# Kernel optimization log

Hardware: AMD Instinct MI355X
Metric: run time of the kernel (lower is better)

## Reference

```python
import jax, jax.numpy as jnp
import numpy as np

EMB = 512
HEADS = 8
WINDOW = 128


def setup_inputs() -> dict:
    key = jax.random.key(0)
    ks = jax.random.split(key, 9)
    s = 1.0 / np.sqrt(EMB)
    x = jax.random.normal(ks[0], (2, 4096, EMB), dtype=jnp.float32)
    mk = lambda k: jax.random.uniform(k, (EMB, EMB), jnp.float32, -s, s)
    mb = lambda k: jax.random.uniform(k, (EMB,), jnp.float32, -s, s)
    return {
        "x": x,
        "Wq": mk(ks[1]), "bq": mb(ks[2]),
        "Wk": mk(ks[3]), "bk": mb(ks[4]),
        "Wv": mk(ks[5]), "bv": mb(ks[6]),
        "Wo": mk(ks[7]), "bo": mb(ks[8]),
    }


def _split_heads(y, b, n):
    # [b, n, emb] -> [b, h, n, d]
    return y.reshape(b, n, HEADS, EMB // HEADS).transpose(0, 2, 1, 3)


def reference(x, Wq, bq, Wk, bk, Wv, bv, Wo, bo):
    b, n, _ = x.shape
    q = _split_heads(x @ Wq.T + bq, b, n)
    k = _split_heads(x @ Wk.T + bk, b, n)
    v = _split_heads(x @ Wv.T + bv, b, n)
    energy = jnp.einsum('bhqd,bhkd->bhqk', q, k)  # [b,h,n,n]
    idx = jnp.arange(n)
    # banded mask: disallowed where |i - j| > window (matches torch loop)
    disallow = jnp.abs(idx[:, None] - idx[None, :]) > WINDOW
    fmin = jnp.float32(np.finfo(np.float32).min)
    energy = jnp.where(disallow[None, None], fmin, energy)
    att = jax.nn.softmax(energy / jnp.float32(np.sqrt(EMB)), axis=-1)
    out = jnp.einsum('bhql,bhld->bhqd', att, v)
    out = out.transpose(0, 2, 1, 3).reshape(b, n, EMB)
    return out @ Wo.T + bo
```

## Files before the change

kernel.cpp:

```cpp
#include <hip/hip_runtime.h>

#define EMB 512
#define HEADS 8
#define HD 64
#define NSEQ 4096
#define BATCH 2
#define WINDOW 128

typedef unsigned short u16;
typedef __attribute__((ext_vector_type(8))) short bf16x8;
typedef __attribute__((ext_vector_type(4))) float f32x4;

#define XS 4194304u
#define WS 262144u
#define BS 512u

__device__ __forceinline__ float bf2f(u16 u) {
    union { unsigned int i; float f; } x;
    x.i = ((unsigned int)u) << 16;
    return x.f;
}

__device__ __forceinline__ u16 f2bf(float f) {
    union { float f; unsigned int i; } x;
    x.f = f;
    unsigned int i = x.i;
    unsigned int lsb = (i >> 16) & 1u;
    i += 0x7fffu + lsb;
    return (u16)(i >> 16);
}

struct raw8 { uint4 lo, hi; };

__device__ __forceinline__ raw8 loadraw8(const void* base, size_t off, int isbf) {
    raw8 r;
    if (isbf) {
        r.lo = *(const uint4*)((const u16*)base + off);
    } else {
        const float* f = (const float*)base + off;
        r.lo = *(const uint4*)f;
        r.hi = *(const uint4*)(f + 4);
    }
    return r;
}

__device__ __forceinline__ uint4 cvt8(const raw8& r, int isbf) {
    if (isbf) return r.lo;
    const float* a = (const float*)&r.lo;
    const float* b = (const float*)&r.hi;
    uint4 o;
    o.x = (unsigned)f2bf(a[0]) | ((unsigned)f2bf(a[1]) << 16);
    o.y = (unsigned)f2bf(a[2]) | ((unsigned)f2bf(a[3]) << 16);
    o.z = (unsigned)f2bf(b[0]) | ((unsigned)f2bf(b[1]) << 16);
    o.w = (unsigned)f2bf(b[2]) | ((unsigned)f2bf(b[3]) << 16);
    return o;
}

__device__ __forceinline__ int probe_bf16(const void* p) {
    const int lane = threadIdx.x & 63;
    u16 w = ((const u16*)p)[lane * 2];
    int e = (w >> 7) & 0xff;
    bool sane = (w == 0) || (e >= 100 && e <= 140);
    unsigned long long m = __ballot(sane);
    return __popcll(m) >= 48;
}

__global__ __launch_bounds__(256)
void prepass(const void* __restrict__ x,
             const void* __restrict__ Wq, const void* __restrict__ bq,
             const void* __restrict__ Wk, const void* __restrict__ bk,
             const void* __restrict__ Wv, const void* __restrict__ bv,
             const void* __restrict__ Wo, const void* __restrict__ bo,
             u16* __restrict__ xb, u16* __restrict__ wb, u16* __restrict__ bb,
             int* __restrict__ flags)
{
    const int fx  = probe_bf16(x);
    const int fwq = probe_bf16(Wq), fbq = probe_bf16(bq);
    const int fwk = probe_bf16(Wk), fbk = probe_bf16(bk);
    const int fwv = probe_bf16(Wv), fbv = probe_bf16(bv);
    const int fwo = probe_bf16(Wo), fbo = probe_bf16(bo);
    if (blockIdx.x == 0 && threadIdx.x == 0) flags[0] = fx;

    size_t idx = ((size_t)blockIdx.x * 256 + threadIdx.x) * 8;
    const size_t T_X = XS, T_W = XS + 4 * (size_t)WS, T_ALL = T_W + 4 * (size_t)BS;
    if (idx >= T_ALL) return;

    const void* src; int fl; u16* dst; size_t off;
    if (idx < T_X) {
        src = x; fl = fx; dst = xb; off = idx;
    } else if (idx < T_W) {
        size_t w = idx - T_X;
        int wi = (int)(w / WS); off = w % WS;
        src = (wi == 0) ? Wq : (wi == 1) ? Wk : (wi == 2) ? Wv : Wo;
        fl  = (wi == 0) ? fwq : (wi == 1) ? fwk : (wi == 2) ? fwv : fwo;
        dst = wb + (size_t)wi * WS;
    } else {
        size_t b = idx - T_W;
        int bi = (int)(b / BS); off = b % BS;
        src = (bi == 0) ? bq : (bi == 1) ? bk : (bi == 2) ? bv : bo;
        fl  = (bi == 0) ? fbq : (bi == 1) ? fbk : (bi == 2) ? fbv : fbo;
        dst = bb + (size_t)bi * BS;
    }
    *(uint4*)(dst + off) = cvt8(loadraw8(src, off, fl), fl);
}

#define TP 136
__global__ __launch_bounds__(256)
void qkv_gemm(const u16* __restrict__ X, const u16* __restrict__ Wall,
              const u16* __restrict__ ball,
              u16* __restrict__ qo, u16* __restrict__ ko, u16* __restrict__ vo)
{
    __shared__ __align__(16) u16 SH[64 * TP];
    u16* As = SH;
    u16* Bs = SH + 4096;

    const int tid  = threadIdx.x;
    const int wave = tid >> 6;
    const int lane = tid & 63;
    const int quad = lane >> 4;
    const int l16  = lane & 15;
    const int wm = wave >> 1, wn = wave & 1;

    const int m0 = blockIdx.x * 128;
    const int by = blockIdx.y;
    const int wsel = by >> 2;
    const int n0 = (by & 3) * 128;

    const u16* W  = Wall + (size_t)wsel * WS;
    const u16* bi = ball + (size_t)wsel * BS;
    u16* out      = (wsel == 0) ? qo : (wsel == 1) ? ko : vo;
    const float oscale = (wsel == 0) ? 0.04419417382415922f : 1.0f;

    f32x4 acc[4][4];
#pragma unroll
    for (int i = 0; i < 4; ++i)
#pragma unroll
        for (int j = 0; j < 4; ++j)
            acc[i][j] = (f32x4){0.f, 0.f, 0.f, 0.f};

    const int c1 = tid, c2 = tid + 256;
    const int r1 = c1 >> 2, k1 = (c1 & 3) * 8;
    const int r2 = c2 >> 2, k2 = (c2 & 3) * 8;

    uint4 a1 = *(const uint4*)(X + (size_t)(m0 + r1) * EMB + k1);
    uint4 a2 = *(const uint4*)(X + (size_t)(m0 + r2) * EMB + k2);
    uint4 b1 = *(const uint4*)(W + (size_t)(n0 + r1) * EMB + k1);
    uint4 b2 = *(const uint4*)(W + (size_t)(n0 + r2) * EMB + k2);

    for (int kt = 0; kt < 16; ++kt) {
        __syncthreads();
        *(uint4*)&As[c1 * 8] = a1;
        *(uint4*)&As[c2 * 8] = a2;
        *(uint4*)&Bs[c1 * 8] = b1;
        *(uint4*)&Bs[c2 * 8] = b2;
        __syncthreads();

        if (kt < 15) {
            const int kk0 = (kt + 1) * 32;
            a1 = *(const uint4*)(X + (size_t)(m0 + r1) * EMB + kk0 + k1);
            a2 = *(const uint4*)(X + (size_t)(m0 + r2) * EMB + kk0 + k2);
            b1 = *(const uint4*)(W + (size_t)(n0 + r1) * EMB + kk0 + k1);
            b2 = *(const uint4*)(W + (size_t)(n0 + r2) * EMB + kk0 + k2);
        }

        bf16x8 af[4], bfr[4];
#pragma unroll
        for (int i = 0; i < 4; ++i)
            af[i] = *(const bf16x8*)&As[(wm * 64 + i * 16 + l16) * 32 + quad * 8];
#pragma unroll
        for (int j = 0; j < 4; ++j)
            bfr[j] = *(const bf16x8*)&Bs[(wn * 64 + j * 16 + l16) * 32 + quad * 8];
#pragma unroll
        for (int i = 0; i < 4; ++i)
#pragma unroll
            for (int j = 0; j < 4; ++j)
                acc[i][j] = __builtin_amdgcn_mfma_f32_16x16x32_bf16(af[i], bfr[j], acc[i][j], 0, 0, 0);
    }

    if (wsel != 2) {
#pragma unroll
        for (int j = 0; j < 4; ++j) {
            const int col = n0 + wn * 64 + j * 16 + l16;
            const float bv_ = bf2f(bi[col]);
            const int h = col >> 6, d = col & 63;
#pragma unroll
            for (int i = 0; i < 4; ++i) {
#pragma unroll
                for (int r = 0; r < 4; ++r) {
                    const int row = m0 + wm * 64 + i * 16 + quad * 4 + r;
                    const int b = row >> 12, n = row & 4095;
                    out[(((size_t)(b * HEADS + h) * NSEQ) + n) * HD + d] =
                        f2bf((acc[i][j][r] + bv_) * oscale);
                }
            }
        }
    } else {
        const int b = m0 >> 12;
        const int nbase = m0 & 4095;
#pragma unroll
        for (int half = 0; half < 2; ++half) {
            __syncthreads();
            if (wn == half) {
#pragma unroll
                for (int j = 0; j < 4; ++j) {
                    const int col = n0 + wn * 64 + j * 16 + l16;
                    const float bv_ = bf2f(bi[col]);
                    const int cl = j * 16 + l16;
#pragma unroll
                    for (int i = 0; i < 4; ++i)
#pragma unroll
                        for (int r = 0; r < 4; ++r) {
                            const int rowl = wm * 64 + i * 16 + quad * 4 + r;
                            SH[cl * TP + rowl] = f2bf(acc[i][j][r] + bv_);
                        }
                }
            }
            __syncthreads();
#pragma unroll
            for (int p = 0; p < 4; ++p) {
                const int idx  = tid + p * 256;
                const int dcol = idx >> 4;
                const int nch  = (idx & 15) * 8;
                uint4 val = *(const uint4*)&SH[dcol * TP + nch];
                const int col = n0 + half * 64 + dcol;
                const int h = col >> 6, d = col & 63;
                *(uint4*)(out + ((size_t)((b * HEADS + h) * HD + d)) * NSEQ + nbase + nch) = val;
            }
        }
    }
}

#define KP 72
__global__ __launch_bounds__(256)
void attn_mfma(const u16* __restrict__ q, const u16* __restrict__ k,
               const u16* __restrict__ v, u16* __restrict__ ao)
{
    __shared__ __align__(16) u16 Ks[64 * KP];
    __shared__ __align__(16) u16 Vt[64 * KP];

    const int tid  = threadIdx.x;
    const int wave = tid >> 6;
    const int lane = tid & 63;
    const int quad = lane >> 4;
    const int l16  = lane & 15;

    const int bh = blockIdx.y;
    const int q0 = blockIdx.x * 64;
    const int qw = q0 + wave * 16;
    const size_t base = (size_t)bh * NSEQ * HD;

    bf16x8 qa0 = *(const bf16x8*)(q + base + (size_t)(qw + l16) * HD + quad * 8);
    bf16x8 qa1 = *(const bf16x8*)(q + base + (size_t)(qw + l16) * HD + 32 + quad * 8);

    f32x4 O[4];
    float m_run = -1e30f, l_run = 0.f;
#pragma unroll
    for (int t = 0; t < 4; ++t) O[t] = (f32x4){0.f, 0.f, 0.f, 0.f};

    const int row_s[2] = { tid >> 3, (tid + 256) >> 3 };
    const int ch8      = (tid & 7) * 8;

    uint4 pkv[2], pvv[2];
    {
        const int kbase = q0 - 128;
        const int koff  = (kbase < 0) ? 0 : (kbase > NSEQ - 64 ? NSEQ - 64 : kbase);
#pragma unroll
        for (int s = 0; s < 2; ++s) {
            int kg = kbase + row_s[s];
            kg = (kg < 0) ? 0 : (kg > NSEQ - 1 ? NSEQ - 1 : kg);
            pkv[s] = *(const uint4*)(k + base + (size_t)kg * HD + ch8);
            pvv[s] = *(const uint4*)(v + base + (size_t)row_s[s] * NSEQ + koff + ch8);
        }
    }

    for (int c = 0; c < 5; ++c) {
        const int kbase = q0 - 128 + c * 64;

        __syncthreads();
#pragma unroll
        for (int s = 0; s < 2; ++s) {
            *(uint4*)&Ks[row_s[s] * KP + ch8] = pkv[s];
            *(uint4*)&Vt[row_s[s] * KP + ch8] = pvv[s];
        }
        __syncthreads();

        if (c < 4) {
            const int kb2  = kbase + 64;
            const int koff = (kb2 < 0) ? 0 : (kb2 > NSEQ - 64 ? NSEQ - 64 : kb2);
#pragma unroll
            for (int s = 0; s < 2; ++s) {
                int kg = kb2 + row_s[s];
                kg = (kg < 0) ? 0 : (kg > NSEQ - 1 ? NSEQ - 1 : kg);
                pkv[s] = *(const uint4*)(k + base + (size_t)kg * HD + ch8);
                pvv[s] = *(const uint4*)(v + base + (size_t)row_s[s] * NSEQ + koff + ch8);
            }
        }

        f32x4 sv[4];
#pragma unroll
        for (int t = 0; t < 4; ++t) {
            bf16x8 b0 = *(const bf16x8*)&Ks[(t * 16 + l16) * KP + quad * 8];
            bf16x8 b1 = *(const bf16x8*)&Ks[(t * 16 + l16) * KP + 32 + quad * 8];
            f32x4 sacc = (f32x4){0.f, 0.f, 0.f, 0.f};
            sacc = __builtin_amdgcn_mfma_f32_16x16x32_bf16(b0, qa0, sacc, 0, 0, 0);
            sacc = __builtin_amdgcn_mfma_f32_16x16x32_bf16(b1, qa1, sacc, 0, 0, 0);
            sv[t] = sacc;
        }

        const int iq = qw + l16;
#pragma unroll
        for (int t = 0; t < 4; ++t) {
#pragma unroll
            for (int r = 0; r < 4; ++r) {
                const int jg = kbase + t * 16 + quad * 4 + r;
                const bool jok = ((unsigned)jg) < (unsigned)NSEQ;
                const bool band = ((unsigned)(iq - jg + WINDOW)) <= (unsigned)(2 * WINDOW);
                if (!(jok && band)) sv[t][r] = -1e30f;
            }
        }

        float mnew = sv[0][0];
#pragma unroll
        for (int t = 0; t < 4; ++t)
#pragma unroll
            for (int r = 0; r < 4; ++r) mnew = fmaxf(mnew, sv[t][r]);
        mnew = fmaxf(mnew, __shfl_xor(mnew, 16, 64));
        mnew = fmaxf(mnew, __shfl_xor(mnew, 32, 64));

        const float mi = fmaxf(m_run, mnew);
        const float alpha = __expf(m_run - mi);
        m_run = mi;

        float p[4][4], lnew = 0.f;
#pragma unroll
        for (int t = 0; t < 4; ++t)
#pragma unroll
            for (int r = 0; r < 4; ++r) {
                float pv = (sv[t][r] > -1e29f) ? __expf(sv[t][r] - mi) : 0.f;
                p[t][r] = pv;
                lnew += pv;
            }
        lnew += __shfl_xor(lnew, 16, 64);
        lnew += __shfl_xor(lnew, 32, 64);
        l_run = l_run * alpha + lnew;

        float alphaO[4];
#pragma unroll
        for (int r = 0; r < 4; ++r)
            alphaO[r] = __shfl(alpha, quad * 4 + r, 64);
#pragma unroll
        for (int t = 0; t < 4; ++t)
#pragma unroll
            for (int r = 0; r < 4; ++r)
                O[t][r] *= alphaO[r];

#pragma unroll
        for (int t = 0; t < 4; ++t) {
            bf16x8 pa;
            pa[0] = (short)f2bf(p[t][0]);
            pa[1] = (short)f2bf(p[t][1]);
            pa[2] = (short)f2bf(p[t][2]);
            pa[3] = (short)f2bf(p[t][3]);
            pa[4] = 0; pa[5] = 0; pa[6] = 0; pa[7] = 0;
#pragma unroll
            for (int t2 = 0; t2 < 4; ++t2) {
                const u16* vp = &Vt[(t2 * 16 + l16) * KP + t * 16 + quad * 4];
                uint2 vlo = *(const uint2*)vp;
                bf16x8 vb;
                *(uint2*)&vb = vlo;
                *((uint2*)&vb + 1) = vlo;
                O[t2] = __builtin_amdgcn_mfma_f32_16x16x32_bf16(pa, vb, O[t2], 0, 0, 0);
            }
        }
    }

    const int bb = bh >> 3, hh = bh & 7;
    const float rli = 1.f / l_run;
    float rlO[4];
#pragma unroll
    for (int r = 0; r < 4; ++r)
        rlO[r] = __shfl(rli, quad * 4 + r, 64);
#pragma unroll
    for (int t = 0; t < 4; ++t)
#pragma unroll
        for (int r = 0; r < 4; ++r) {
            const int iq2 = qw + quad * 4 + r;
            ao[((size_t)(bb * NSEQ + iq2)) * EMB + hh * HD + t * 16 + l16] =
                f2bf(O[t][r] * rlO[r]);
        }
}

__global__ __launch_bounds__(256)
void out_gemm(const u16* __restrict__ A, const u16* __restrict__ W,
              const u16* __restrict__ bias, void* __restrict__ out,
              const int* __restrict__ flags)
{
    __shared__ __align__(16) u16 As[128 * 32];
    __shared__ __align__(16) u16 Bs[128 * 32];

    const int tid  = threadIdx.x;
    const int wave = tid >> 6;
    const int lane = tid & 63;
    const int quad = lane >> 4;
    const int l16  = lane & 15;
    const int wm = wave >> 1, wn = wave & 1;

    const int m0 = blockIdx.x * 128;
    const int n0 = blockIdx.y * 128;
    const int fo = flags[0];

    f32x4 acc[4][4];
#pragma unroll
    for (int i = 0; i < 4; ++i)
#pragma unroll
        for (int j = 0; j < 4; ++j)
            acc[i][j] = (f32x4){0.f, 0.f, 0.f, 0.f};

    const int c1 = tid, c2 = tid + 256;
    const int r1 = c1 >> 2, k1 = (c1 & 3) * 8;
    const int r2 = c2 >> 2, k2 = (c2 & 3) * 8;

    uint4 a1 = *(const uint4*)(A + (size_t)(m0 + r1) * EMB + k1);
    uint4 a2 = *(const uint4*)(A + (size_t)(m0 + r2) * EMB + k2);
    uint4 b1 = *(const uint4*)(W + (size_t)(n0 + r1) * EMB + k1);
    uint4 b2 = *(const uint4*)(W + (size_t)(n0 + r2) * EMB + k2);

    for (int kt = 0; kt < 16; ++kt) {
        __syncthreads();
        *(uint4*)&As[c1 * 8] = a1;
        *(uint4*)&As[c2 * 8] = a2;
        *(uint4*)&Bs[c1 * 8] = b1;
        *(uint4*)&Bs[c2 * 8] = b2;
        __syncthreads();

        if (kt < 15) {
            const int kk0 = (kt + 1) * 32;
            a1 = *(const uint4*)(A + (size_t)(m0 + r1) * EMB + kk0 + k1);
            a2 = *(const uint4*)(A + (size_t)(m0 + r2) * EMB + kk0 + k2);
            b1 = *(const uint4*)(W + (size_t)(n0 + r1) * EMB + kk0 + k1);
            b2 = *(const uint4*)(W + (size_t)(n0 + r2) * EMB + kk0 + k2);
        }

        bf16x8 af[4], bfr[4];
#pragma unroll
        for (int i = 0; i < 4; ++i)
            af[i] = *(const bf16x8*)&As[(wm * 64 + i * 16 + l16) * 32 + quad * 8];
#pragma unroll
        for (int j = 0; j < 4; ++j)
            bfr[j] = *(const bf16x8*)&Bs[(wn * 64 + j * 16 + l16) * 32 + quad * 8];
#pragma unroll
        for (int i = 0; i < 4; ++i)
#pragma unroll
            for (int j = 0; j < 4; ++j)
                acc[i][j] = __builtin_amdgcn_mfma_f32_16x16x32_bf16(af[i], bfr[j], acc[i][j], 0, 0, 0);
    }

#pragma unroll
    for (int j = 0; j < 4; ++j) {
        const int col = n0 + wn * 64 + j * 16 + l16;
        const float bv_ = bf2f(bias[col]);
#pragma unroll
        for (int i = 0; i < 4; ++i) {
#pragma unroll
            for (int r = 0; r < 4; ++r) {
                const int row = m0 + wm * 64 + i * 16 + quad * 4 + r;
                const float val = acc[i][j][r] + bv_;
                const size_t idx = (size_t)row * EMB + col;
                if (fo) ((u16*)out)[idx] = f2bf(val);
                else    ((float*)out)[idx] = val;
            }
        }
    }
}

extern "C" void kernel_launch(void* const* d_in, const int* in_sizes, int n_in,
                              void* d_out, int out_size, void* d_ws, size_t ws_size,
                              hipStream_t stream)
{
    const size_t HSZ  = (size_t)BATCH * HEADS * NSEQ * HD;
    char* base = (char*)d_ws;
    int* flags = (int*)base;
    const size_t off = 256;

    u16* xb = (u16*)(base + off);
    u16* wb = xb + XS;
    u16* bb = wb + 4 * (size_t)WS;
    u16* kk = bb + 4 * (size_t)BS;
    u16* vv = kk + HSZ;
    u16* ao = vv + HSZ;
    u16* qq = ao + HSZ;

    const size_t need_t1 = off + 2 * (XS + 4 * (size_t)WS + 4 * (size_t)BS + 4 * HSZ);
    if (ws_size < need_t1) {
        qq = (u16*)d_out;
    }

    prepass<<<dim3(2561), 256, 0, stream>>>(d_in[0], d_in[1], d_in[2], d_in[3],
                                            d_in[4], d_in[5], d_in[6], d_in[7],
                                            d_in[8], xb, wb, bb, flags);
    qkv_gemm<<<dim3(64, 12), 256, 0, stream>>>(xb, wb, bb, qq, kk, vv);
    attn_mfma<<<dim3(64, 16), 256, 0, stream>>>(qq, kk, vv, ao);
    out_gemm<<<dim3(64, 4), 256, 0, stream>>>(ao, wb + 3 * (size_t)WS, bb + 3 * (size_t)BS,
                                              d_out, flags);
}
```

Measured before the change: 169.0 us.

## Drop LDS staging; load MFMA operands directly from global in GEMMs and attention

The QKV and output GEMMs no longer stage A/B tiles through shared memory with block barriers. Each wave now loads its MFMA fragments straight from global memory, with partial unrolling to overlap the loads. The attention kernel likewise reads K rows and transposed V directly from global, with clamped indices, instead of cooperative LDS tiles. This removes the barriers and LDS traffic but makes waves re-fetch data they previously shared, so it leans on the L1/L2 caches and issues more, narrower global loads (notably 8-byte V reads).

```diff
diff --git a/kernel.cpp b/kernel.cpp
--- a/kernel.cpp
+++ b/kernel.cpp
@@ -111,8 +111,6 @@
               u16* __restrict__ qo, u16* __restrict__ ko, u16* __restrict__ vo)
 {
     __shared__ __align__(16) u16 SH[64 * TP];
-    u16* As = SH;
-    u16* Bs = SH + 4096;
 
     const int tid  = threadIdx.x;
     const int wave = tid >> 6;
@@ -138,38 +136,25 @@
         for (int j = 0; j < 4; ++j)
             acc[i][j] = (f32x4){0.f, 0.f, 0.f, 0.f};
 
-    const int c1 = tid, c2 = tid + 256;
-    const int r1 = c1 >> 2, k1 = (c1 & 3) * 8;
-    const int r2 = c2 >> 2, k2 = (c2 & 3) * 8;
-
-    uint4 a1 = *(const uint4*)(X + (size_t)(m0 + r1) * EMB + k1);
-    uint4 a2 = *(const uint4*)(X + (size_t)(m0 + r2) * EMB + k2);
-    uint4 b1 = *(const uint4*)(W + (size_t)(n0 + r1) * EMB + k1);
-    uint4 b2 = *(const uint4*)(W + (size_t)(n0 + r2) * EMB + k2);
-
+    const u16* Arow[4];
+    const u16* Brow[4];
+#pragma unroll
+    for (int i = 0; i < 4; ++i)
+        Arow[i] = X + (size_t)(m0 + wm * 64 + i * 16 + l16) * EMB + quad * 8;
+#pragma unroll
+    for (int j = 0; j < 4; ++j)
+        Brow[j] = W + (size_t)(n0 + wn * 64 + j * 16 + l16) * EMB + quad * 8;
+
+#pragma unroll 4
     for (int kt = 0; kt < 16; ++kt) {
-        __syncthreads();
-        *(uint4*)&As[c1 * 8] = a1;
-        *(uint4*)&As[c2 * 8] = a2;
-        *(uint4*)&Bs[c1 * 8] = b1;
-        *(uint4*)&Bs[c2 * 8] = b2;
-        __syncthreads();
-
-        if (kt < 15) {
-            const int kk0 = (kt + 1) * 32;
-            a1 = *(const uint4*)(X + (size_t)(m0 + r1) * EMB + kk0 + k1);
-            a2 = *(const uint4*)(X + (size_t)(m0 + r2) * EMB + kk0 + k2);
-            b1 = *(const uint4*)(W + (size_t)(n0 + r1) * EMB + kk0 + k1);
-            b2 = *(const uint4*)(W + (size_t)(n0 + r2) * EMB + kk0 + k2);
-        }
-
+        const int kk0 = kt * 32;
         bf16x8 af[4], bfr[4];
 #pragma unroll
         for (int i = 0; i < 4; ++i)
-            af[i] = *(const bf16x8*)&As[(wm * 64 + i * 16 + l16) * 32 + quad * 8];
+            af[i] = *(const bf16x8*)(Arow[i] + kk0);
 #pragma unroll
         for (int j = 0; j < 4; ++j)
-            bfr[j] = *(const bf16x8*)&Bs[(wn * 64 + j * 16 + l16) * 32 + quad * 8];
+            bfr[j] = *(const bf16x8*)(Brow[j] + kk0);
 #pragma unroll
         for (int i = 0; i < 4; ++i)
 #pragma unroll
@@ -230,14 +215,10 @@
     }
 }
 
-#define KP 72
 __global__ __launch_bounds__(256)
 void attn_mfma(const u16* __restrict__ q, const u16* __restrict__ k,
                const u16* __restrict__ v, u16* __restrict__ ao)
 {
-    __shared__ __align__(16) u16 Ks[64 * KP];
-    __shared__ __align__(16) u16 Vt[64 * KP];
-
     const int tid  = threadIdx.x;
     const int wave = tid >> 6;
     const int lane = tid & 63;
@@ -257,50 +238,18 @@
 #pragma unroll
     for (int t = 0; t < 4; ++t) O[t] = (f32x4){0.f, 0.f, 0.f, 0.f};
 
-    const int row_s[2] = { tid >> 3, (tid + 256) >> 3 };
-    const int ch8      = (tid & 7) * 8;
-
-    uint4 pkv[2], pvv[2];
-    {
-        const int kbase = q0 - 128;
-        const int koff  = (kbase < 0) ? 0 : (kbase > NSEQ - 64 ? NSEQ - 64 : kbase);
-#pragma unroll
-        for (int s = 0; s < 2; ++s) {
-            int kg = kbase + row_s[s];
-            kg = (kg < 0) ? 0 : (kg > NSEQ - 1 ? NSEQ - 1 : kg);
-            pkv[s] = *(const uint4*)(k + base + (size_t)kg * HD + ch8);
-            pvv[s] = *(const uint4*)(v + base + (size_t)row_s[s] * NSEQ + koff + ch8);
-        }
-    }
-
+#pragma unroll 1
     for (int c = 0; c < 5; ++c) {
         const int kbase = q0 - 128 + c * 64;
 
-        __syncthreads();
-#pragma unroll
-        for (int s = 0; s < 2; ++s) {
-            *(uint4*)&Ks[row_s[s] * KP + ch8] = pkv[s];
-            *(uint4*)&Vt[row_s[s] * KP + ch8] = pvv[s];
-        }
-        __syncthreads();
-
-        if (c < 4) {
-            const int kb2  = kbase + 64;
-            const int koff = (kb2 < 0) ? 0 : (kb2 > NSEQ - 64 ? NSEQ - 64 : kb2);
-#pragma unroll
-            for (int s = 0; s < 2; ++s) {
-                int kg = kb2 + row_s[s];
-                kg = (kg < 0) ? 0 : (kg > NSEQ - 1 ? NSEQ - 1 : kg);
-                pkv[s] = *(const uint4*)(k + base + (size_t)kg * HD + ch8);
-                pvv[s] = *(const uint4*)(v + base + (size_t)row_s[s] * NSEQ + koff + ch8);
-            }
-        }
-
         f32x4 sv[4];
 #pragma unroll
         for (int t = 0; t < 4; ++t) {
-            bf16x8 b0 = *(const bf16x8*)&Ks[(t * 16 + l16) * KP + quad * 8];
-            bf16x8 b1 = *(const bf16x8*)&Ks[(t * 16 + l16) * KP + 32 + quad * 8];
+            int kg = kbase + t * 16 + l16;
+            kg = (kg < 0) ? 0 : (kg > NSEQ - 1 ? NSEQ - 1 : kg);
+            const u16* kp = k + base + (size_t)kg * HD;
+            bf16x8 b0 = *(const bf16x8*)(kp + quad * 8);
+            bf16x8 b1 = *(const bf16x8*)(kp + 32 + quad * 8);
             f32x4 sacc = (f32x4){0.f, 0.f, 0.f, 0.f};
             sacc = __builtin_amdgcn_mfma_f32_16x16x32_bf16(b0, qa0, sacc, 0, 0, 0);
             sacc = __builtin_amdgcn_mfma_f32_16x16x32_bf16(b1, qa1, sacc, 0, 0, 0);
@@ -362,9 +311,11 @@
             pa[2] = (short)f2bf(p[t][2]);
             pa[3] = (short)f2bf(p[t][3]);
             pa[4] = 0; pa[5] = 0; pa[6] = 0; pa[7] = 0;
+            int ko = kbase + t * 16 + quad * 4;
+            ko = (ko < 0) ? 0 : (ko > NSEQ - 4 ? NSEQ - 4 : ko);
 #pragma unroll
             for (int t2 = 0; t2 < 4; ++t2) {
-                const u16* vp = &Vt[(t2 * 16 + l16) * KP + t * 16 + quad * 4];
+                const u16* vp = v + base + (size_t)(t2 * 16 + l16) * NSEQ + ko;
                 uint2 vlo = *(const uint2*)vp;
                 bf16x8 vb;
                 *(uint2*)&vb = vlo;
@@ -395,9 +346,6 @@
               const u16* __restrict__ bias, void* __restrict__ out,
               const int* __restrict__ flags)
 {
-    __shared__ __align__(16) u16 As[128 * 32];
-    __shared__ __align__(16) u16 Bs[128 * 32];
-
     const int tid  = threadIdx.x;
     const int wave = tid >> 6;
     const int lane = tid & 63;
@@ -416,38 +364,25 @@
         for (int j = 0; j < 4; ++j)
             acc[i][j] = (f32x4){0.f, 0.f, 0.f, 0.f};
 
-    const int c1 = tid, c2 = tid + 256;
-    const int r1 = c1 >> 2, k1 = (c1 & 3) * 8;
-    const int r2 = c2 >> 2, k2 = (c2 & 3) * 8;
-
-    uint4 a1 = *(const uint4*)(A + (size_t)(m0 + r1) * EMB + k1);
-    uint4 a2 = *(const uint4*)(A + (size_t)(m0 + r2) * EMB + k2);
-    uint4 b1 = *(const uint4*)(W + (size_t)(n0 + r1) * EMB + k1);
-    uint4 b2 = *(const uint4*)(W + (size_t)(n0 + r2) * EMB + k2);
-
+    const u16* Arow[4];
+    const u16* Brow[4];
+#pragma unroll
+    for (int i = 0; i < 4; ++i)
+        Arow[i] = A + (size_t)(m0 + wm * 64 + i * 16 + l16) * EMB + quad * 8;
+#pragma unroll
+    for (int j = 0; j < 4; ++j)
+        Brow[j] = W + (size_t)(n0 + wn * 64 + j * 16 + l16) * EMB + quad * 8;
+
+#pragma unroll 4
     for (int kt = 0; kt < 16; ++kt) {
-        __syncthreads();
-        *(uint4*)&As[c1 * 8] = a1;
-        *(uint4*)&As[c2 * 8] = a2;
-        *(uint4*)&Bs[c1 * 8] = b1;
-        *(uint4*)&Bs[c2 * 8] = b2;
-        __syncthreads();
-
-        if (kt < 15) {
-            const int kk0 = (kt + 1) * 32;
-            a1 = *(const uint4*)(A + (size_t)(m0 + r1) * EMB + kk0 + k1);
-            a2 = *(const uint4*)(A + (size_t)(m0 + r2) * EMB + kk0 + k2);
-            b1 = *(const uint4*)(W + (size_t)(n0 + r1) * EMB + kk0 + k1);
-            b2 = *(const uint4*)(W + (size_t)(n0 + r2) * EMB + kk0 + k2);
-        }
-
+        const int kk0 = kt * 32;
         bf16x8 af[4], bfr[4];
 #pragma unroll
         for (int i = 0; i < 4; ++i)
-            af[i] = *(const bf16x8*)&As[(wm * 64 + i * 16 + l16) * 32 + quad * 8];
+            af[i] = *(const bf16x8*)(Arow[i] + kk0);
 #pragma unroll
         for (int j = 0; j < 4; ++j)
-            bfr[j] = *(const bf16x8*)&Bs[(wn * 64 + j * 16 + l16) * 32 + quad * 8];
+            bfr[j] = *(const bf16x8*)(Brow[j] + kk0);
 #pragma unroll
         for (int i = 0; i < 4; ++i)
 #pragma unroll
```

Result: slower. 219.4 us (+29.8%).
